# Optimization experiments

Hardware: AMD Instinct MI355X
Metric: run time of the kernel (lower is better)

The kernel has to match this reference:

```python
import jax, jax.numpy as jnp
from jax import lax
import numpy as np

D = 1024      # input_size
H = D // 2    # proj hidden
T = 25        # num_ner_labels
B, S = 64, 512


def setup_inputs() -> dict:
    key = jax.random.key(0)
    ks = jax.random.split(key, 8)
    sc1 = 1.0 / np.sqrt(D)
    sc2 = 1.0 / np.sqrt(H)
    return {
        "encoder_out": jax.random.normal(ks[0], (B, S, D), dtype=jnp.float32),
        "W1": jax.random.uniform(ks[1], (D, H), jnp.float32, -sc1, sc1),
        "b1": jax.random.uniform(ks[2], (H,), jnp.float32, -sc1, sc1),
        "W2": jax.random.uniform(ks[3], (H, T), jnp.float32, -sc2, sc2),
        "b2": jax.random.uniform(ks[4], (T,), jnp.float32, -sc2, sc2),
        "start_trans": jax.random.uniform(ks[5], (T,), jnp.float32, -0.1, 0.1),
        "end_trans": jax.random.uniform(ks[6], (T,), jnp.float32, -0.1, 0.1),
        "trans": jax.random.uniform(ks[7], (T, T), jnp.float32, -0.1, 0.1),
        "ner_labels": jax.random.randint(jax.random.fold_in(key, 1), (B, S), 0, T, dtype=jnp.int64),
        "mask": jnp.ones((B, S), dtype=bool),
    }


def _crf_nll(emissions, start_trans, end_trans, trans, labels, mask):
    # torchcrf negative mean log-likelihood, batch_first
    maskf = mask.astype(emissions.dtype)
    # numerator: score of gold path
    em_at_tag = jnp.take_along_axis(emissions, labels[..., None], axis=2)[..., 0]  # [B,S]
    score0 = start_trans[labels[:, 0]] + em_at_tag[:, 0]
    trans_sc = trans[labels[:, :-1], labels[:, 1:]]                                # [B,S-1]
    step_score = (trans_sc + em_at_tag[:, 1:]) * maskf[:, 1:]
    last_idx = mask.sum(axis=1).astype(jnp.int32) - 1
    last_tag = jnp.take_along_axis(labels, last_idx[:, None].astype(labels.dtype), axis=1)[:, 0]
    numerator = score0 + step_score.sum(axis=1) + end_trans[last_tag]
    # denominator: log partition via forward algorithm (scan over time)
    alpha0 = start_trans[None, :] + emissions[:, 0]                                # [B,T]
    em_rest = jnp.swapaxes(emissions[:, 1:], 0, 1)                                 # [S-1,B,T]
    m_rest = jnp.swapaxes(mask[:, 1:], 0, 1)                                       # [S-1,B]

    def step(alpha, xs):
        em_t, m_t = xs
        new = jax.scipy.special.logsumexp(
            alpha[:, :, None] + trans[None, :, :] + em_t[:, None, :], axis=1)
        return jnp.where(m_t[:, None], new, alpha), None

    alpha, _ = lax.scan(step, alpha0, (em_rest, m_rest))
    log_Z = jax.scipy.special.logsumexp(alpha + end_trans[None, :], axis=1)        # [B]
    return -jnp.mean(numerator - log_Z)


def reference(encoder_out, W1, b1, W2, b2, start_trans, end_trans, trans, ner_labels, mask):
    h = jax.nn.gelu(encoder_out @ W1 + b1, approximate=False)  # dropout is eval-mode identity
    emissions = h @ W2 + b2                                    # [B,S,T]
    return _crf_nll(emissions, start_trans, end_trans, trans, ner_labels, mask)
```

## Files before the change

### kernel.cpp

```cpp
#include <hip/hip_runtime.h>
#include <math.h>

#define DD 1024
#define HH 512
#define TT 25
#define BB 64
#define SS 512
#define MM (BB*SS)
#define NC 32

typedef __attribute__((ext_vector_type(8))) short short8;
typedef __attribute__((ext_vector_type(4))) float floatx4;
typedef __attribute__((ext_vector_type(16))) float floatx16;

static __device__ __forceinline__ unsigned short f2bf(float f) {
  unsigned u = __float_as_uint(f);
  u = (u + 0x7FFFu + ((u >> 16) & 1u)) >> 16;
  return (unsigned short)u;
}
static __device__ __forceinline__ float rl(float v, int i) {
  return __int_as_float(__builtin_amdgcn_readlane(__float_as_int(v), i));
}
static __device__ __forceinline__ void load_lds16(const void* g, void* l) {
  __builtin_amdgcn_global_load_lds(
      (const __attribute__((address_space(1))) unsigned int*)g,
      (__attribute__((address_space(3))) unsigned int*)l, 16, 0, 0);
}
union U4S8 { uint4 u; short8 s; };

__global__ __launch_bounds__(256) void k_prep(
    const float* __restrict__ W1, const float* __restrict__ W2,
    unsigned short* __restrict__ W1T2, unsigned short* __restrict__ W2p) {
  const int t = threadIdx.x;
  if (blockIdx.y < 8) {
    __shared__ unsigned short tile[64 * 72];
    const int k0 = blockIdx.x * 64, n0 = blockIdx.y * 64;
    #pragma unroll
    for (int it = 0; it < 16; it++) {
      int idx = t + it * 256;
      int kk = idx >> 6, nn = idx & 63;
      tile[nn * 72 + kk] = f2bf(W1[(size_t)(k0 + kk) * HH + n0 + nn]);
    }
    __syncthreads();
    #pragma unroll
    for (int it = 0; it < 4; it++) {
      int idx = (t + it * 256) * 4;
      int nn = idx >> 6, kk = idx & 63;
      ushort4 v;
      v.x = tile[nn * 72 + kk];     v.y = tile[nn * 72 + kk + 1];
      v.z = tile[nn * 72 + kk + 2]; v.w = tile[nn * 72 + kk + 3];
      int kt = (k0 >> 5) + (kk >> 5), kkk = kk & 31;
      int n = n0 + nn;
      size_t slice = (size_t)kt * (HH * 32) + (size_t)(n & ~63) * 32;
      int o = ((((n & 63) * 64) + ((kkk >> 3) * 16)) ^ ((n & 7) << 4)) + (kkk & 7) * 2;
      *(ushort4*)((char*)W1T2 + slice * 2 + o) = v;
    }
  } else {
    #pragma unroll
    for (int e = 0; e < 4; e++) {
      int idx = blockIdx.x * 1024 + t + e * 256;
      int row = idx >> 9, k = idx & 511;
      float v = (row < TT) ? W2[(size_t)k * TT + row] : 0.f;
      W2p[(size_t)row * HH + k] = f2bf(v);
    }
  }
}

__global__ __launch_bounds__(256, 4) void k_emis(
    const float* __restrict__ X, const unsigned short* __restrict__ W1T2,
    const float* __restrict__ b1, const unsigned short* __restrict__ W2p,
    const float* __restrict__ b2, float* __restrict__ em) {
  __shared__ __attribute__((aligned(16))) short lds[18432];

  const int tid  = threadIdx.x;
  const int lane = tid & 63;
  const int w    = tid >> 6;
  const int l15  = lane & 15;
  const int kc   = lane >> 4;
  const int m0   = blockIdx.x * 64;
  const int colbase = blockIdx.y * 256;

  floatx4 acc[4][4];
  #pragma unroll
  for (int a = 0; a < 4; a++)
    #pragma unroll
    for (int b = 0; b < 4; b++)
      acc[a][b] = (floatx4){0.f, 0.f, 0.f, 0.f};

  const int am = tid >> 2;
  const int ac = tid & 3;
  const float* Xrow = X + (size_t)(m0 + am) * DD + ac * 8;
  const int xwb = (am * 64 + ac * 16) ^ ((am & 7) << 4);

  const unsigned short* gW = W1T2 + (size_t)(colbase + w * 64) * 32 + lane * 8;

  {
    short* lW = lds + 2048 + w * 2048;
    #pragma unroll
    for (int j = 0; j < 4; j++)
      load_lds16(gW + j * 512, lW + j * 512);
  }
  float4 xa0 = *(const float4*)(Xrow);
  float4 xa1 = *(const float4*)(Xrow + 4);
  float4 xb0 = *(const float4*)(Xrow + 32);
  float4 xb1 = *(const float4*)(Xrow + 36);

  for (int t = 0; t < 32; ++t) {
    short* sBc = lds + 2048 + (t & 1) * 8192;

    float4 xc0, xc1;
    if (t < 31) {
      short* lW = lds + 2048 + ((t + 1) & 1) * 8192 + w * 2048;
      const unsigned short* g = gW + (size_t)(t + 1) * (HH * 32);
      #pragma unroll
      for (int j = 0; j < 4; j++)
        load_lds16(g + j * 512, lW + j * 512);
    }
    if (t < 30) {
      xc0 = *(const float4*)(Xrow + (t + 2) * 32);
      xc1 = *(const float4*)(Xrow + (t + 2) * 32 + 4);
    }

    {
      unsigned p0 = (unsigned)f2bf(xa0.x) | ((unsigned)f2bf(xa0.y) << 16);
      unsigned p1 = (unsigned)f2bf(xa0.z) | ((unsigned)f2bf(xa0.w) << 16);
      unsigned p2 = (unsigned)f2bf(xa1.x) | ((unsigned)f2bf(xa1.y) << 16);
      unsigned p3 = (unsigned)f2bf(xa1.z) | ((unsigned)f2bf(xa1.w) << 16);
      *(uint4*)((char*)lds + xwb) = make_uint4(p0, p1, p2, p3);
    }
    xa0 = xb0; xa1 = xb1;
    if (t < 30) { xb0 = xc0; xb1 = xc1; }

    if (t < 31) {
      asm volatile("s_waitcnt vmcnt(6) lgkmcnt(0)" ::: "memory");
    } else {
      asm volatile("s_waitcnt vmcnt(0) lgkmcnt(0)" ::: "memory");
    }
    __builtin_amdgcn_s_barrier();
    asm volatile("" ::: "memory");

    short8 af[4], bfr[4];
    #pragma unroll
    for (int mt = 0; mt < 4; mt++) {
      int row = mt * 16 + l15;
      af[mt] = *(const short8*)((char*)lds + ((row * 64 + kc * 16) ^ ((l15 & 7) << 4)));
    }
    #pragma unroll
    for (int nt = 0; nt < 4; nt++) {
      int rloc = nt * 16 + l15;
      int off = (rloc * 64 + kc * 16) ^ ((l15 & 7) << 4);
      bfr[nt] = *(const short8*)((char*)(sBc + w * 2048) + off);
    }
    asm volatile("s_waitcnt lgkmcnt(0)" ::: "memory");
    __builtin_amdgcn_sched_barrier(0);
    #pragma unroll
    for (int mt = 0; mt < 4; mt++)
      #pragma unroll
      for (int nt = 0; nt < 4; nt++)
        acc[mt][nt] = __builtin_amdgcn_mfma_f32_16x16x32_bf16(af[mt], bfr[nt], acc[mt][nt], 0, 0, 0);

    asm volatile("" ::: "memory");
    __builtin_amdgcn_s_barrier();
    asm volatile("" ::: "memory");
  }

  short* sH = lds;
  float* sC = (float*)(lds + 8448);
  const int mt_g = w & 1, kh_g = w >> 1;

  short8 w2f[2][4];
  #pragma unroll
  for (int nt2 = 0; nt2 < 2; nt2++)
    #pragma unroll
    for (int ks = 0; ks < 4; ks++)
      w2f[nt2][ks] = *(const short8*)(W2p + (size_t)(nt2 * 16 + l15) * HH
                                      + colbase + kh_g * 128 + ks * 32 + kc * 8);

  #pragma unroll
  for (int half = 0; half < 2; half++) {
    __syncthreads();
    #pragma unroll
    for (int mt2 = 0; mt2 < 2; mt2++) {
      int mt = half * 2 + mt2;
      #pragma unroll
      for (int nt = 0; nt < 4; nt++) {
        int n = w * 64 + nt * 16 + l15;
        float bias = b1[colbase + n];
        #pragma unroll
        for (int r = 0; r < 4; r++) {
          int ml = mt2 * 16 + kc * 4 + r;
          float v = acc[mt][nt][r] + bias;
          float g = 0.5f * v * (1.0f + erff(v * 0.70710678118654752f));
          sH[ml * 264 + n] = (short)f2bf(g);
        }
      }
    }
    __syncthreads();
    #pragma unroll
    for (int nt2 = 0; nt2 < 2; nt2++) {
      floatx4 c2 = (floatx4){0.f, 0.f, 0.f, 0.f};
      #pragma unroll
      for (int ks = 0; ks < 4; ks++) {
        short8 a2 = *(const short8*)(sH + (mt_g * 16 + l15) * 264 + kh_g * 128 + ks * 32 + kc * 8);
        c2 = __builtin_amdgcn_mfma_f32_16x16x32_bf16(a2, w2f[nt2][ks], c2, 0, 0, 0);
      }
      #pragma unroll
      for (int r = 0; r < 4; r++)
        sC[kh_g * 1024 + (mt_g * 16 + kc * 4 + r) * 32 + nt2 * 16 + l15] = c2[r];
    }
    __syncthreads();
    for (int o = tid; o < 32 * TT; o += 256) {
      int m = o / TT, t = o % TT;
      float val = sC[m * 32 + t] + sC[1024 + m * 32 + t];
      if (blockIdx.y == 0) val += b2[t];
      atomicAdd(em + (size_t)(m0 + half * 32 + m) * TT + t, val);
    }
  }
}

__global__ __launch_bounds__(64) void k_chunk(
    const float* __restrict__ em, const float* __restrict__ trans,
    float* __restrict__ Mats) {
  const int b = blockIdx.x, c = blockIdx.y;
  const int lane = threadIdx.x;
  const int h = lane >> 5;
  const int n = lane & 31;
  const float* emb = em + (size_t)b * SS * TT;

  unsigned a1p[4], a2p[4];
  #pragma unroll
  for (int p = 0; p < 4; p++) {
    int i0 = h * 8 + 2 * p, i1 = i0 + 1;
    unsigned lo = (n < TT && i0 < TT) ? (unsigned)f2bf(__expf(trans[i0 * TT + n])) : 0u;
    unsigned hi = (n < TT && i1 < TT) ? (unsigned)f2bf(__expf(trans[i1 * TT + n])) : 0u;
    a1p[p] = lo | (hi << 16);
    int j0 = 16 + h * 8 + 2 * p, j1 = j0 + 1;
    lo = (n < TT && j0 < TT) ? (unsigned)f2bf(__expf(trans[j0 * TT + n])) : 0u;
    hi = (n < TT && j1 < TT) ? (unsigned)f2bf(__expf(trans[j1 * TT + n])) : 0u;
    a2p[p] = lo | (hi << 16);
  }
  U4S8 A1, A2;
  A1.u = make_uint4(a1p[0], a1p[1], a1p[2], a1p[3]);
  A2.u = make_uint4(a2p[0], a2p[1], a2p[2], a2p[3]);

  unsigned bp1[4], bp2[4];
  #pragma unroll
  for (int p = 0; p < 4; p++) {
    int k0 = h * 8 + 2 * p;
    bp1[p] = ((k0 == n) ? 0x3F80u : 0u) | ((k0 + 1 == n) ? 0x3F800000u : 0u);
    int k2 = 16 + h * 8 + 2 * p;
    bp2[p] = ((k2 == n) ? 0x3F80u : 0u) | ((k2 + 1 == n) ? 0x3F800000u : 0u);
  }

  const int s0 = 1 + c * 16;
  const int nst = (s0 + 16 <= SS) ? 16 : (SS - s0);

  float emv[16], f[16];
  #pragma unroll
  for (int e = 0; e < 16; e++) {
    int r = (e & 3) + 8 * (e >> 2) + 4 * h;
    emv[e] = (r < TT) ? emb[s0 * TT + r] : 0.f;
  }

  for (int t = 0; t < nst; t++) {
    const float rs = (t == 8) ? 32.0f : 0.0f;
    float ex[16];
    #pragma unroll
    for (int e = 0; e < 16; e++) ex[e] = __expf(emv[e] - rs);
    int sn = (s0 + t + 1 < SS) ? s0 + t + 1 : SS - 1;
    #pragma unroll
    for (int e = 0; e < 16; e++) {
      int r = (e & 3) + 8 * (e >> 2) + 4 * h;
      emv[e] = (r < TT) ? emb[sn * TT + r] : 0.f;
    }
    U4S8 B1, B2;
    B1.u = make_uint4(bp1[0], bp1[1], bp1[2], bp1[3]);
    B2.u = make_uint4(bp2[0], bp2[1], bp2[2], bp2[3]);
    floatx16 D = __builtin_amdgcn_mfma_f32_32x32x16_bf16(A1.s, B1.s,
                   __builtin_amdgcn_mfma_f32_32x32x16_bf16(A2.s, B2.s,
                     (floatx16){0.f,0.f,0.f,0.f,0.f,0.f,0.f,0.f,
                                0.f,0.f,0.f,0.f,0.f,0.f,0.f,0.f}, 0,0,0), 0,0,0);
    #pragma unroll
    for (int e = 0; e < 16; e++) f[e] = D[e] * ex[e];
    if (t == nst - 1) break;
    unsigned P[16];
    #pragma unroll
    for (int p = 0; p < 8; p++)
      P[p] = (unsigned)f2bf(f[2 * p]) | ((unsigned)f2bf(f[2 * p + 1]) << 16);
    unsigned sp[8];
    #pragma unroll
    for (int p = 0; p < 8; p++)
      sp[p] = (unsigned)__shfl_xor((int)P[p], 32);
    bool up = (h == 1);
    bp1[0] = up ? sp[2] : P[0];
    bp1[1] = up ? sp[3] : P[1];
    bp1[2] = up ? P[2] : sp[0];
    bp1[3] = up ? P[3] : sp[1];
    bp2[0] = up ? sp[6] : P[4];
    bp2[1] = up ? sp[7] : P[5];
    bp2[2] = up ? P[6] : sp[4];
    bp2[3] = up ? P[7] : sp[5];
  }

  if (n < TT) {
    float* Mc = Mats + ((size_t)(b * NC + c)) * (TT * TT) + n * TT;
    #pragma unroll
    for (int e = 0; e < 16; e++) {
      int r = (e & 3) + 8 * (e >> 2) + 4 * h;
      if (r < TT) Mc[r] = __logf(f[e]) + 32.0f;
    }
  }
}

__global__ __launch_bounds__(64) void k_comb(
    const float* __restrict__ em, const float* __restrict__ start,
    const float* __restrict__ endt, const float* __restrict__ trans,
    const int* __restrict__ labels, const float* __restrict__ Mats,
    float* __restrict__ partial) {
  const int b = blockIdx.x;
  const int tid = threadIdx.x;
  const float* emb = em + (size_t)b * SS * TT;
  const int* lab = labels + b * SS;

  float part = 0.f;
  for (int s = tid; s < SS; s += 64) {
    int l = lab[s];
    if (s == 0) part += start[l] + emb[l];
    else        part += trans[lab[s - 1] * TT + l] + emb[s * TT + l];
  }
  #pragma unroll
  for (int off = 32; off; off >>= 1) part += __shfl_xor(part, off);
  float num = part + endt[lab[SS - 1]];

  const int jj = (tid < TT) ? tid : 0;
  float a = (tid < TT) ? start[tid] + emb[tid] : -1e30f;
  const float* Mb = Mats + (size_t)b * NC * (TT * TT);
  for (int c = 0; c < NC; c++) {
    const float* Mc = Mb + c * (TT * TT);
    float col[TT];
    float mxc = -1e30f;
    #pragma unroll
    for (int i = 0; i < TT; i++) {
      col[i] = Mc[i * TT + jj];
      mxc = fmaxf(mxc, col[i]);
    }
    float a0 = __builtin_amdgcn_readfirstlane(a);
    float p = __expf(a - a0);
    float d0 = 0.f, d1 = 0.f, d2 = 0.f, d3 = 0.f;
    #pragma unroll
    for (int i = 0; i < 24; i += 4) {
      d0 = fmaf(rl(p, i + 0), __expf(col[i + 0] - mxc), d0);
      d1 = fmaf(rl(p, i + 1), __expf(col[i + 1] - mxc), d1);
      d2 = fmaf(rl(p, i + 2), __expf(col[i + 2] - mxc), d2);
      d3 = fmaf(rl(p, i + 3), __expf(col[i + 3] - mxc), d3);
    }
    d0 = fmaf(rl(p, 24), __expf(col[24] - mxc), d0);
    float anew = a0 + mxc + __logf((d0 + d1) + (d2 + d3));
    a = (tid < TT) ? anew : -1e30f;
  }

  float v = (tid < TT) ? a + endt[tid] : -1e30f;
  float mx = v;
  #pragma unroll
  for (int off = 16; off; off >>= 1) mx = fmaxf(mx, __shfl_xor(mx, off, 32));
  float e = (tid < TT) ? __expf(v - mx) : 0.f;
  #pragma unroll
  for (int off = 16; off; off >>= 1) e += __shfl_xor(e, off, 32);
  if (tid == 0) partial[b] = (mx + __logf(e)) - num;
}

__global__ void k_final(const float* __restrict__ partial, float* __restrict__ out) {
  int tid = threadIdx.x;
  float v = partial[tid];
  #pragma unroll
  for (int off = 32; off; off >>= 1) v += __shfl_xor(v, off);
  if (tid == 0) out[0] = v * (1.0f / 64.0f);
}

extern "C" void kernel_launch(void* const* d_in, const int* in_sizes, int n_in,
                              void* d_out, int out_size, void* d_ws, size_t ws_size,
                              hipStream_t stream) {
  const float* X   = (const float*)d_in[0];
  const float* W1  = (const float*)d_in[1];
  const float* b1  = (const float*)d_in[2];
  const float* W2  = (const float*)d_in[3];
  const float* b2  = (const float*)d_in[4];
  const float* st  = (const float*)d_in[5];
  const float* en  = (const float*)d_in[6];
  const float* tr  = (const float*)d_in[7];
  const int* labels = (const int*)d_in[8];

  char* ws = (char*)d_ws;
  unsigned short* W1T2 = (unsigned short*)ws;
  unsigned short* W2p  = (unsigned short*)(ws + 0x100000);
  float* em            = (float*)(ws + 0x110000);
  float* Mats          = (float*)(ws + 0x430000);
  float* partial       = (float*)(ws + 0x930000);

  k_prep <<<dim3(16, 9), 256, 0, stream>>>(W1, W2, W1T2, W2p);
  hipMemsetAsync(em, 0, (size_t)MM * TT * sizeof(float), stream);
  k_emis <<<dim3(512, 2), 256, 0, stream>>>(X, W1T2, b1, W2p, b2, em);
  k_chunk<<<dim3(BB, NC), 64, 0, stream>>>(em, tr, Mats);
  k_comb <<<BB, 64, 0, stream>>>(em, st, en, tr, labels, Mats, partial);
  k_final<<<1, 64, 0, stream>>>(partial, (float*)d_out);
}
```

Before: 304.8 us.

## Replace emission atomics with split partial buffers and prefetch chunk matrices

The emission kernel now writes each column-half's partial emissions to a separate buffer with plain stores instead of atomicAdd into a zeroed buffer. This removes the memset and the atomic traffic, and consumers sum the two halves on read. The 1D grid interleaves the two column halves of each row tile so they run close together. The chunk kernel packs four chunks per 256-thread block, and the combine kernel double-buffers chunk-matrix columns to hide load latency in its serial loop. The cost is twice the emission storage and an extra load on every emission read.

Measured after the change: 311.7 us. 2.3% more time.

```diff
diff --git a/kernel.cpp b/kernel.cpp
--- a/kernel.cpp
+++ b/kernel.cpp
@@ -8,6 +8,7 @@
 #define SS 512
 #define MM (BB*SS)
 #define NC 32
+#define EMPL ((size_t)MM * TT)
 
 typedef __attribute__((ext_vector_type(8))) short short8;
 typedef __attribute__((ext_vector_type(4))) float floatx4;
@@ -77,8 +78,10 @@
   const int w    = tid >> 6;
   const int l15  = lane & 15;
   const int kc   = lane >> 4;
-  const int m0   = blockIdx.x * 64;
-  const int colbase = blockIdx.y * 256;
+  const int bid  = blockIdx.x;
+  const int yb   = bid & 1;
+  const int m0   = (bid >> 1) * 64;
+  const int colbase = yb * 256;
 
   floatx4 acc[4][4];
   #pragma unroll
@@ -167,6 +170,7 @@
   short* sH = lds;
   float* sC = (float*)(lds + 8448);
   const int mt_g = w & 1, kh_g = w >> 1;
+  float* emp = em + (size_t)yb * EMPL;
 
   short8 w2f[2][4];
   #pragma unroll
@@ -212,20 +216,22 @@
     for (int o = tid; o < 32 * TT; o += 256) {
       int m = o / TT, t = o % TT;
       float val = sC[m * 32 + t] + sC[1024 + m * 32 + t];
-      if (blockIdx.y == 0) val += b2[t];
-      atomicAdd(em + (size_t)(m0 + half * 32 + m) * TT + t, val);
-    }
-  }
-}
-
-__global__ __launch_bounds__(64) void k_chunk(
+      if (yb == 0) val += b2[t];
+      emp[(size_t)(m0 + half * 32 + m) * TT + t] = val;
+    }
+  }
+}
+
+__global__ __launch_bounds__(256) void k_chunk(
     const float* __restrict__ em, const float* __restrict__ trans,
     float* __restrict__ Mats) {
-  const int b = blockIdx.x, c = blockIdx.y;
-  const int lane = threadIdx.x;
+  const int b = blockIdx.x;
+  const int c = blockIdx.y * 4 + (threadIdx.x >> 6);
+  const int lane = threadIdx.x & 63;
   const int h = lane >> 5;
   const int n = lane & 31;
-  const float* emb = em + (size_t)b * SS * TT;
+  const float* e0 = em + (size_t)b * SS * TT;
+  const float* e1 = e0 + EMPL;
 
   unsigned a1p[4], a2p[4];
   #pragma unroll
@@ -259,7 +265,7 @@
   #pragma unroll
   for (int e = 0; e < 16; e++) {
     int r = (e & 3) + 8 * (e >> 2) + 4 * h;
-    emv[e] = (r < TT) ? emb[s0 * TT + r] : 0.f;
+    emv[e] = (r < TT) ? (e0[s0 * TT + r] + e1[s0 * TT + r]) : 0.f;
   }
 
   for (int t = 0; t < nst; t++) {
@@ -271,7 +277,7 @@
     #pragma unroll
     for (int e = 0; e < 16; e++) {
       int r = (e & 3) + 8 * (e >> 2) + 4 * h;
-      emv[e] = (r < TT) ? emb[sn * TT + r] : 0.f;
+      emv[e] = (r < TT) ? (e0[sn * TT + r] + e1[sn * TT + r]) : 0.f;
     }
     U4S8 B1, B2;
     B1.u = make_uint4(bp1[0], bp1[1], bp1[2], bp1[3]);
@@ -312,6 +318,26 @@
   }
 }
 
+static __device__ __forceinline__ float foldchunk(
+    const float* col, float a, int tid) {
+  float mxc = -1e30f;
+  #pragma unroll
+  for (int i = 0; i < TT; i++) mxc = fmaxf(mxc, col[i]);
+  float a0 = __builtin_amdgcn_readfirstlane(a);
+  float p = __expf(a - a0);
+  float d0 = 0.f, d1 = 0.f, d2 = 0.f, d3 = 0.f;
+  #pragma unroll
+  for (int i = 0; i < 24; i += 4) {
+    d0 = fmaf(rl(p, i + 0), __expf(col[i + 0] - mxc), d0);
+    d1 = fmaf(rl(p, i + 1), __expf(col[i + 1] - mxc), d1);
+    d2 = fmaf(rl(p, i + 2), __expf(col[i + 2] - mxc), d2);
+    d3 = fmaf(rl(p, i + 3), __expf(col[i + 3] - mxc), d3);
+  }
+  d0 = fmaf(rl(p, 24), __expf(col[24] - mxc), d0);
+  float anew = a0 + mxc + __logf((d0 + d1) + (d2 + d3));
+  return (tid < TT) ? anew : -1e30f;
+}
+
 __global__ __launch_bounds__(64) void k_comb(
     const float* __restrict__ em, const float* __restrict__ start,
     const float* __restrict__ endt, const float* __restrict__ trans,
@@ -319,44 +345,38 @@
     float* __restrict__ partial) {
   const int b = blockIdx.x;
   const int tid = threadIdx.x;
-  const float* emb = em + (size_t)b * SS * TT;
+  const float* e0 = em + (size_t)b * SS * TT;
+  const float* e1 = e0 + EMPL;
   const int* lab = labels + b * SS;
 
   float part = 0.f;
   for (int s = tid; s < SS; s += 64) {
     int l = lab[s];
-    if (s == 0) part += start[l] + emb[l];
-    else        part += trans[lab[s - 1] * TT + l] + emb[s * TT + l];
+    if (s == 0) part += start[l] + (e0[l] + e1[l]);
+    else        part += trans[lab[s - 1] * TT + l] + (e0[s * TT + l] + e1[s * TT + l]);
   }
   #pragma unroll
   for (int off = 32; off; off >>= 1) part += __shfl_xor(part, off);
   float num = part + endt[lab[SS - 1]];
 
   const int jj = (tid < TT) ? tid : 0;
-  float a = (tid < TT) ? start[tid] + emb[tid] : -1e30f;
+  float a = (tid < TT) ? start[tid] + (e0[tid] + e1[tid]) : -1e30f;
   const float* Mb = Mats + (size_t)b * NC * (TT * TT);
-  for (int c = 0; c < NC; c++) {
-    const float* Mc = Mb + c * (TT * TT);
-    float col[TT];
-    float mxc = -1e30f;
-    #pragma unroll
-    for (int i = 0; i < TT; i++) {
-      col[i] = Mc[i * TT + jj];
-      mxc = fmaxf(mxc, col[i]);
-    }
-    float a0 = __builtin_amdgcn_readfirstlane(a);
-    float p = __expf(a - a0);
-    float d0 = 0.f, d1 = 0.f, d2 = 0.f, d3 = 0.f;
-    #pragma unroll
-    for (int i = 0; i < 24; i += 4) {
-      d0 = fmaf(rl(p, i + 0), __expf(col[i + 0] - mxc), d0);
-      d1 = fmaf(rl(p, i + 1), __expf(col[i + 1] - mxc), d1);
-      d2 = fmaf(rl(p, i + 2), __expf(col[i + 2] - mxc), d2);
-      d3 = fmaf(rl(p, i + 3), __expf(col[i + 3] - mxc), d3);
-    }
-    d0 = fmaf(rl(p, 24), __expf(col[24] - mxc), d0);
-    float anew = a0 + mxc + __logf((d0 + d1) + (d2 + d3));
-    a = (tid < TT) ? anew : -1e30f;
+
+  float cA[TT], cB[TT];
+  #pragma unroll
+  for (int i = 0; i < TT; i++) cA[i] = Mb[i * TT + jj];
+  for (int c = 0; c < NC; c += 2) {
+    const float* M1 = Mb + (size_t)(c + 1) * (TT * TT);
+    #pragma unroll
+    for (int i = 0; i < TT; i++) cB[i] = M1[i * TT + jj];
+    a = foldchunk(cA, a, tid);
+    if (c + 2 < NC) {
+      const float* M2 = Mb + (size_t)(c + 2) * (TT * TT);
+      #pragma unroll
+      for (int i = 0; i < TT; i++) cA[i] = M2[i * TT + jj];
+    }
+    a = foldchunk(cB, a, tid);
   }
 
   float v = (tid < TT) ? a + endt[tid] : -1e30f;
@@ -394,13 +414,12 @@
   unsigned short* W1T2 = (unsigned short*)ws;
   unsigned short* W2p  = (unsigned short*)(ws + 0x100000);
   float* em            = (float*)(ws + 0x110000);
-  float* Mats          = (float*)(ws + 0x430000);
-  float* partial       = (float*)(ws + 0x930000);
+  float* Mats          = (float*)(ws + 0x750000);
+  float* partial       = (float*)(ws + 0xC40000);
 
   k_prep <<<dim3(16, 9), 256, 0, stream>>>(W1, W2, W1T2, W2p);
-  hipMemsetAsync(em, 0, (size_t)MM * TT * sizeof(float), stream);
-  k_emis <<<dim3(512, 2), 256, 0, stream>>>(X, W1T2, b1, W2p, b2, em);
-  k_chunk<<<dim3(BB, NC), 64, 0, stream>>>(em, tr, Mats);
+  k_emis <<<1024, 256, 0, stream>>>(X, W1T2, b1, W2p, b2, em);
+  k_chunk<<<dim3(BB, 8), 256, 0, stream>>>(em, tr, Mats);
   k_comb <<<BB, 64, 0, stream>>>(em, st, en, tr, labels, Mats, partial);
   k_final<<<1, 64, 0, stream>>>(partial, (float*)d_out);
 }
```
